# Kernel optimization log

Measured on AMD Instinct MI355X. Metric: run time of the kernel, lower is better.

Reference implementation:

```python
import jax, jax.numpy as jnp
import numpy as np

B, N, NP, NS = 8, 4096, 1024, 32
CF = 64            # input point-feature channels; in_channel = 3 + CF = 67
MLP = [64, 128, 256]
EPS = 1e-5         # BatchNorm eps (torch default)


def setup_inputs() -> dict:
    key = jax.random.key(0)
    ks = jax.random.split(key, 8)
    inp = {
        "xyz": jax.random.normal(ks[0], (B, N, 3), jnp.float32),
        "points": jax.random.normal(ks[1], (B, CF, N), jnp.float32),
        "sample_idx": jax.random.randint(ks[2], (B, NP), 0, N, dtype=jnp.int32),
        "neighbor_idx": jax.random.randint(ks[3], (B, NP, NS), 0, N, dtype=jnp.int32),
    }
    c = 3 + CF
    for i, o in enumerate(MLP):
        wk = jax.random.fold_in(ks[4], i)
        inp[f"W{i}"] = jax.random.normal(wk, (o, c), jnp.float32) * (1.0 / np.sqrt(c))
        inp[f"b{i}"] = jnp.zeros((o,), jnp.float32)
        inp[f"gamma{i}"] = jnp.ones((o,), jnp.float32)
        inp[f"beta{i}"] = jnp.zeros((o,), jnp.float32)
        c = o
    return inp


def _forward(xyz, points, sample_idx, neighbor_idx, params):
    # xyz: (B,N,3)  points: (B,CF,N)
    new_xyz = jnp.take_along_axis(xyz, sample_idx[:, :, None], axis=1)        # (B,NP,3)
    nbr_xyz = jax.vmap(lambda x, idx: x[idx])(xyz, neighbor_idx)               # (B,NP,NS,3)
    rel = nbr_xyz - new_xyz[:, :, None, :]                                     # (B,NP,NS,3)
    nbr_feat = jax.vmap(lambda f, idx: f[:, idx])(points, neighbor_idx)        # (B,CF,NP,NS)
    x = jnp.concatenate([rel.transpose(0, 3, 1, 2), nbr_feat], axis=1)         # (B,3+CF,NP,NS)
    # 1x1 Conv2d -> BatchNorm2d (training-mode batch stats) -> ReLU stack
    for W, b, g, be in params:
        x = jnp.einsum('oc,bcps->bops', W, x) + b[None, :, None, None]
        mu = x.mean(axis=(0, 2, 3), keepdims=True)
        var = x.var(axis=(0, 2, 3), keepdims=True)
        x = g[None, :, None, None] * (x - mu) * jax.lax.rsqrt(var + EPS) + be[None, :, None, None]
        x = jax.nn.relu(x)
    new_points = x.max(axis=-1)                                                # (B,C_out,NP)
    return new_xyz, new_points


def reference(xyz, points, sample_idx, neighbor_idx,
              W0, b0, gamma0, beta0,
              W1, b1, gamma1, beta1,
              W2, b2, gamma2, beta2):
    params = [(W0, b0, gamma0, beta0), (W1, b1, gamma1, beta1), (W2, b2, gamma2, beta2)]
    return _forward(xyz, points, sample_idx, neighbor_idx, params)
```

## Files before the change

kernel.cpp:

```cpp
#include <hip/hip_runtime.h>

typedef unsigned short u16;
typedef unsigned int u32;
typedef __attribute__((ext_vector_type(8))) short short8;
typedef __attribute__((ext_vector_type(16))) float f32x16;

#define BB 8
#define NN 4096
#define NPP 1024
#define NSS 32
#define CFF 64
#define C0 67
#define H0 64
#define H1 128
#define H2 256
#define MTOT (BB*NPP*NSS)
#define BN_EPS 1e-5f
#define INV_M (1.0f/262144.0f)

#define MFMA32(a,b,c) __builtin_amdgcn_mfma_f32_32x32x16_bf16(a,b,c,0,0,0)

__device__ __forceinline__ float bf2f(u16 h){ return __uint_as_float(((u32)h)<<16); }
__device__ __forceinline__ u16 f2bf(float f){
  u32 u = __float_as_uint(f);
  u32 r = (u + 0x7fffu + ((u>>16)&1u)) >> 16;
  return (u16)r;
}
__device__ __forceinline__ u32 pack2(float a, float b){
  return (u32)f2bf(a) | ((u32)f2bf(b)<<16);
}

#define WS_NEED 46280704u

__global__ __launch_bounds__(256) void k_setup(
    const float* __restrict__ xyz, const float* __restrict__ points,
    const int* __restrict__ sidx,
    const float* __restrict__ W0, const float* __restrict__ W1, const float* __restrict__ W2,
    u16* __restrict__ ptsT, u16* __restrict__ Wt0c, u16* __restrict__ Wt1c,
    u16* __restrict__ Wt2c, float* __restrict__ out_newxyz)
{
  int blk = blockIdx.x, tid = threadIdx.x;
  if (blk < 512) {
    __shared__ float t[64][65];
    int b = blk >> 6, n0 = (blk & 63) << 6;
    int nloc = tid & 63, cpart = tid >> 6;
    for (int i = 0; i < 16; ++i) {
      int c = i*4 + cpart;
      t[c][nloc] = points[(size_t)(b*CFF + c)*NN + n0 + nloc];
    }
    __syncthreads();
    int cloc = tid & 63, npart = tid >> 6;
    for (int i = 0; i < 16; ++i) {
      int n = i*4 + npart;
      ptsT[((size_t)(b*NN + n0 + n))*CFF + cloc] = f2bf(t[cloc][n]);
    }
  } else if (blk < 544) {
    int t0 = (blk - 512)*256 + tid;
    int b = t0 >> 10;
    int s = sidx[t0];
    for (int k = 0; k < 3; ++k)
      out_newxyz[(size_t)t0*3 + k] = xyz[((size_t)(b*NN + s))*3 + k];
  } else if (blk == 544) {
    for (int i = 0; i < 24; ++i) {
      int e = i*256 + tid;
      int kc = e >> 9, o = (e >> 3) & 63, j = e & 7, k = kc*8 + j;
      float v = (k < 64) ? W0[o*C0 + 3 + k] : ((k < 67) ? W0[o*C0 + (k - 64)] : 0.f);
      Wt0c[e] = f2bf(v);
    }
  } else if (blk == 545) {
    for (int i = 0; i < 32; ++i) {
      int e = i*256 + tid;
      int kc = e >> 10, n = (e >> 3) & 127, j = e & 7;
      Wt1c[e] = f2bf(W1[n*H0 + kc*8 + j]);
    }
  } else {
    int base = (blk - 546) * 4096;
    for (int i = 0; i < 16; ++i) {
      int e = base + i*256 + tid;
      int kc = e >> 11, n = (e >> 3) & 255, j = e & 7;
      Wt2c[e] = f2bf(W2[n*H1 + kc*8 + j]);
    }
  }
}

__global__ __launch_bounds__(256) void k_xyz_only(
    const float* __restrict__ xyz, const int* __restrict__ sidx, float* __restrict__ out_newxyz)
{
  int t0 = blockIdx.x*256 + threadIdx.x;
  int b = t0 >> 10;
  int s = sidx[t0];
  for (int k = 0; k < 3; ++k)
    out_newxyz[(size_t)t0*3 + k] = xyz[((size_t)(b*NN + s))*3 + k];
}

__global__ __launch_bounds__(256) void k_l0(
    const float* __restrict__ xyz, const int* __restrict__ sidx, const int* __restrict__ nidx,
    const u16* __restrict__ ptsT, const u16* __restrict__ Wt0c,
    u16* __restrict__ y0, float* __restrict__ stats)
{
  __shared__ u16 XLc[12*128*8];
  __shared__ u16 W0c[12*64*8];
  int tid = threadIdx.x;
  int m0 = blockIdx.x * 128;
  int b = m0 >> 15;

  for (int i = 0; i < 3; ++i)
    ((uint4*)W0c)[i*256 + tid] = ((const uint4*)Wt0c)[i*256 + tid];

  int pos = tid & 127, half = tid >> 7;
  int m = m0 + pos;
  int nb = nidx[m];
  {
    const uint4* prow = (const uint4*)(ptsT + ((size_t)(b*NN + nb))*CFF + half*32);
    uint4 h0 = prow[0], h1 = prow[1], h2 = prow[2], h3 = prow[3];
    *(uint4*)&XLc[((half*4+0)*128 + pos)*8] = h0;
    *(uint4*)&XLc[((half*4+1)*128 + pos)*8] = h1;
    *(uint4*)&XLc[((half*4+2)*128 + pos)*8] = h2;
    *(uint4*)&XLc[((half*4+3)*128 + pos)*8] = h3;
    if (half == 0) {
      int p = (m & 32767) >> 5;
      int sp = sidx[b*NPP + p];
      float r0 = xyz[((size_t)(b*NN+nb))*3+0] - xyz[((size_t)(b*NN+sp))*3+0];
      float r1 = xyz[((size_t)(b*NN+nb))*3+1] - xyz[((size_t)(b*NN+sp))*3+1];
      float r2 = xyz[((size_t)(b*NN+nb))*3+2] - xyz[((size_t)(b*NN+sp))*3+2];
      uint4 v = { pack2(r0, r1), pack2(r2, 0.f), 0u, 0u };
      *(uint4*)&XLc[(8*128 + pos)*8] = v;
    } else {
      uint4 z = {0u,0u,0u,0u};
      *(uint4*)&XLc[(9*128 + pos)*8]  = z;
      *(uint4*)&XLc[(10*128 + pos)*8] = z;
      *(uint4*)&XLc[(11*128 + pos)*8] = z;
    }
  }
  __syncthreads();

  int lane = tid & 63, wv = tid >> 6;
  int l31 = lane & 31, kh = lane >> 5;
  int nt = wv & 1, mtb = (wv >> 1) * 2;
  f32x16 acc[2];
  for (int mi = 0; mi < 2; ++mi) for (int r = 0; r < 16; ++r) acc[mi][r] = 0.f;

  for (int kt = 0; kt < 6; ++kt) {
    int ck = kt*2 + kh;
    short8 bfrag = *(const short8*)&W0c[(ck*64 + nt*32 + l31)*8];
    for (int mi = 0; mi < 2; ++mi) {
      short8 afrag = *(const short8*)&XLc[(ck*128 + (mtb+mi)*32 + l31)*8];
      acc[mi] = MFMA32(afrag, bfrag, acc[mi]);
    }
  }

  float s = 0.f, q = 0.f;
  for (int mi = 0; mi < 2; ++mi)
    for (int r = 0; r < 16; ++r) { float y = acc[mi][r]; s += y; q += y*y; }
  s += __shfl_xor(s, 32); q += __shfl_xor(q, 32);
  if (lane < 32) {
    int slot = blockIdx.x & 7;
    atomicAdd(&stats[slot*256 + nt*32 + lane], s);
    atomicAdd(&stats[2048 + slot*256 + nt*32 + lane], q);
  }
  for (int mi = 0; mi < 2; ++mi)
    for (int r = 0; r < 16; ++r) {
      int mm = (mtb+mi)*32 + (r&3) + 8*(r>>2) + 4*kh;
      y0[(size_t)(m0+mm)*H0 + nt*32 + l31] = f2bf(acc[mi][r]);
    }
}

__global__ __launch_bounds__(256) void k_l1s(
    const u16* __restrict__ y0, const u16* __restrict__ Wt1c,
    const float* __restrict__ g0, const float* __restrict__ e0,
    const float* __restrict__ stIn, float* __restrict__ stOut)
{
  __shared__ u16 X0c[8*128*8];
  __shared__ u16 W1c[8*128*8];
  __shared__ float scl0[64], sft0[64];
  int tid = threadIdx.x;
  int m0 = blockIdx.x * 128;

  if (tid < 64) {
    float s = 0.f, q = 0.f;
    for (int sl = 0; sl < 8; ++sl) { s += stIn[sl*256 + tid]; q += stIn[2048 + sl*256 + tid]; }
    float mu = s*INV_M, var = q*INV_M - mu*mu;
    float sc = g0[tid] * rsqrtf(var + BN_EPS);
    scl0[tid] = sc; sft0[tid] = e0[tid] - mu*sc;
  }
  for (int i = 0; i < 4; ++i)
    ((uint4*)W1c)[i*256 + tid] = ((const uint4*)Wt1c)[i*256 + tid];

  int pos = tid & 127, half = tid >> 7;
  {
    const u16* row = y0 + (size_t)(m0 + pos)*H0 + half*32;
    u16 hs[32];
    for (int t = 0; t < 4; ++t) *(uint4*)&hs[t*8] = ((const uint4*)row)[t];
    __syncthreads();
    u16 ob[32];
    for (int j = 0; j < 32; ++j) {
      int c = half*32 + j;
      ob[j] = f2bf(fmaxf(fmaf(scl0[c], bf2f(hs[j]), sft0[c]), 0.f));
    }
    for (int t = 0; t < 4; ++t)
      *(uint4*)&X0c[((half*4+t)*128 + pos)*8] = *(uint4*)&ob[t*8];
  }
  __syncthreads();

  int lane = tid & 63, wv = tid >> 6;
  int l31 = lane & 31, kh = lane >> 5;
  f32x16 acc[4];
  for (int mt = 0; mt < 4; ++mt) for (int r = 0; r < 16; ++r) acc[mt][r] = 0.f;

  for (int kt = 0; kt < 4; ++kt) {
    int ck = kt*2 + kh;
    short8 bfrag = *(const short8*)&W1c[(ck*128 + wv*32 + l31)*8];
    for (int mt = 0; mt < 4; ++mt) {
      short8 afrag = *(const short8*)&X0c[(ck*128 + mt*32 + l31)*8];
      acc[mt] = MFMA32(afrag, bfrag, acc[mt]);
    }
  }

  float s = 0.f, q = 0.f;
  for (int mt = 0; mt < 4; ++mt)
    for (int r = 0; r < 16; ++r) { float y = acc[mt][r]; s += y; q += y*y; }
  s += __shfl_xor(s, 32); q += __shfl_xor(q, 32);
  if (lane < 32) {
    int slot = blockIdx.x & 7;
    atomicAdd(&stOut[slot*256 + wv*32 + lane], s);
    atomicAdd(&stOut[2048 + slot*256 + wv*32 + lane], q);
  }
}

__global__ __launch_bounds__(256) void k_l2f(
    const u16* __restrict__ y0, const u16* __restrict__ Wt1c, const u16* __restrict__ Wt2c,
    const float* __restrict__ g0, const float* __restrict__ e0,
    const float* __restrict__ g1, const float* __restrict__ e1,
    const float* __restrict__ st0, const float* __restrict__ st1, float* __restrict__ stOut,
    u16* __restrict__ mxp, u16* __restrict__ mnp)
{
  __shared__ u16 X1c[16*64*8];
  __shared__ u16 UB[16384];
  __shared__ float scl0[64], sft0[64], scl1[128], sft1[128];
  int tid = threadIdx.x;
  int m0 = blockIdx.x * 64;

  if (tid < 64) {
    float s = 0.f, q = 0.f;
    for (int sl = 0; sl < 8; ++sl) { s += st0[sl*256 + tid]; q += st0[2048 + sl*256 + tid]; }
    float mu = s*INV_M, var = q*INV_M - mu*mu;
    float sc = g0[tid] * rsqrtf(var + BN_EPS);
    scl0[tid] = sc; sft0[tid] = e0[tid] - mu*sc;
  }
  if (tid < 128) {
    float s = 0.f, q = 0.f;
    for (int sl = 0; sl < 8; ++sl) { s += st1[sl*256 + tid]; q += st1[2048 + sl*256 + tid]; }
    float mu = s*INV_M, var = q*INV_M - mu*mu;
    float sc = g1[tid] * rsqrtf(var + BN_EPS);
    scl1[tid] = sc; sft1[tid] = e1[tid] - mu*sc;
  }
  u16* X0c = UB;
  u16* W1c = UB + 4096;
  for (int i = 0; i < 4; ++i)
    ((uint4*)W1c)[i*256 + tid] = ((const uint4*)Wt1c)[i*256 + tid];

  int pos = tid & 63, grp = tid >> 6;
  {
    const u16* row = y0 + (size_t)(m0 + pos)*H0 + grp*16;
    u16 hs[16];
    *(uint4*)&hs[0] = ((const uint4*)row)[0];
    *(uint4*)&hs[8] = ((const uint4*)row)[1];
    __syncthreads();
    u16 ob[16];
    for (int j = 0; j < 16; ++j) {
      int c = grp*16 + j;
      ob[j] = f2bf(fmaxf(fmaf(scl0[c], bf2f(hs[j]), sft0[c]), 0.f));
    }
    *(uint4*)&X0c[((2*grp)*64 + pos)*8]   = *(uint4*)&ob[0];
    *(uint4*)&X0c[((2*grp+1)*64 + pos)*8] = *(uint4*)&ob[8];
  }
  __syncthreads();

  int lane = tid & 63, wv = tid >> 6;
  int l31 = lane & 31, kh = lane >> 5;

  f32x16 acc1[2];
  for (int mt = 0; mt < 2; ++mt) for (int r = 0; r < 16; ++r) acc1[mt][r] = 0.f;
  for (int kt = 0; kt < 4; ++kt) {
    int ck = kt*2 + kh;
    short8 bfrag = *(const short8*)&W1c[(ck*128 + wv*32 + l31)*8];
    for (int mt = 0; mt < 2; ++mt) {
      short8 afrag = *(const short8*)&X0c[(ck*64 + mt*32 + l31)*8];
      acc1[mt] = MFMA32(afrag, bfrag, acc1[mt]);
    }
  }

  {
    int ch = wv*32 + l31;
    int cb = ch >> 3, cr = ch & 7;
    float sc1 = scl1[ch], sf1 = sft1[ch];
    for (int mt = 0; mt < 2; ++mt)
      for (int r = 0; r < 16; ++r) {
        int mm = mt*32 + (r&3) + 8*(r>>2) + 4*kh;
        X1c[(cb*64 + mm)*8 + cr] = f2bf(fmaxf(fmaf(sc1, acc1[mt][r], sf1), 0.f));
      }
  }
  __syncthreads();

  f32x16 acc2[2][2];
  for (int nt = 0; nt < 2; ++nt) for (int mt = 0; mt < 2; ++mt)
    for (int r = 0; r < 16; ++r) acc2[nt][mt][r] = 0.f;

  for (int h = 0; h < 2; ++h) {
    for (int i = 0; i < 8; ++i)
      ((uint4*)UB)[i*256 + tid] = ((const uint4*)Wt2c)[h*2048 + i*256 + tid];
    __syncthreads();
    for (int k4 = 0; k4 < 4; ++k4) {
      int ckx = (h*4 + k4)*2 + kh;
      int ckw = k4*2 + kh;
      short8 a[2], bf_[2];
      for (int mt = 0; mt < 2; ++mt) a[mt]  = *(const short8*)&X1c[(ckx*64 + mt*32 + l31)*8];
      for (int nt = 0; nt < 2; ++nt) bf_[nt] = *(const short8*)&UB[(ckw*256 + wv*64 + nt*32 + l31)*8];
      for (int nt = 0; nt < 2; ++nt)
        for (int mt = 0; mt < 2; ++mt)
          acc2[nt][mt] = MFMA32(a[mt], bf_[nt], acc2[nt][mt]);
    }
    __syncthreads();
  }

  int slot = blockIdx.x & 7;
  for (int nt = 0; nt < 2; ++nt) {
    float s = 0.f, q = 0.f;
    float mx[2] = {-3.0e38f, -3.0e38f}, mn[2] = {3.0e38f, 3.0e38f};
    for (int mt = 0; mt < 2; ++mt)
      for (int r = 0; r < 16; ++r) {
        float y = acc2[nt][mt][r];
        s += y; q += y*y;
        mx[mt] = fmaxf(mx[mt], y); mn[mt] = fminf(mn[mt], y);
      }
    s += __shfl_xor(s, 32); q += __shfl_xor(q, 32);
    mx[0] = fmaxf(mx[0], __shfl_xor(mx[0], 32));
    mx[1] = fmaxf(mx[1], __shfl_xor(mx[1], 32));
    mn[0] = fminf(mn[0], __shfl_xor(mn[0], 32));
    mn[1] = fminf(mn[1], __shfl_xor(mn[1], 32));
    if (lane < 32) {
      int c = wv*64 + nt*32 + lane;
      atomicAdd(&stOut[slot*256 + c], s);
      atomicAdd(&stOut[2048 + slot*256 + c], q);
      for (int mt = 0; mt < 2; ++mt) {
        size_t pr = (size_t)blockIdx.x*2 + mt;
        mxp[pr*H2 + c] = f2bf(mx[mt]);
        mnp[pr*H2 + c] = f2bf(mn[mt]);
      }
    }
  }
}

__global__ __launch_bounds__(256) void k_final(
    const u16* __restrict__ mxp, const u16* __restrict__ mnp,
    const float* __restrict__ gma, const float* __restrict__ bta,
    const float* __restrict__ stIn, float* __restrict__ out_np)
{
  __shared__ float tmp[256][33];
  int tid = threadIdx.x;
  int b = blockIdx.x >> 5;
  int p0 = (blockIdx.x & 31) * 32;

  float s = 0.f, q = 0.f;
  for (int sl = 0; sl < 8; ++sl) { s += stIn[sl*256 + tid]; q += stIn[2048 + sl*256 + tid]; }
  float mu = s*INV_M, var = q*INV_M - mu*mu;
  float sc = gma[tid] * rsqrtf(var + BN_EPS);
  float sh = bta[tid] - mu*sc;

  for (int pp = 0; pp < 32; ++pp) {
    size_t base = ((size_t)(b*NPP + p0 + pp))*H2 + tid;
    float xv = bf2f(mxp[base]), nv = bf2f(mnp[base]);
    float v = (sc >= 0.f) ? fmaf(sc, xv, sh) : fmaf(sc, nv, sh);
    tmp[tid][pp] = fmaxf(v, 0.f);
  }
  __syncthreads();

  int pl = tid & 31, cg = tid >> 5;
  for (int cc = 0; cc < 32; ++cc) {
    int c = cc*8 + cg;
    out_np[((size_t)b*H2 + c)*NPP + p0 + pl] = tmp[c][pl];
  }
}

extern "C" void kernel_launch(void* const* d_in, const int* in_sizes, int n_in,
                              void* d_out, int out_size, void* d_ws, size_t ws_size,
                              hipStream_t stream)
{
  const float* xyz    = (const float*)d_in[0];
  const float* points = (const float*)d_in[1];
  const int*   sidx   = (const int*)d_in[2];
  const int*   nidx   = (const int*)d_in[3];
  const float* W0 = (const float*)d_in[4];
  const float* g0 = (const float*)d_in[6];
  const float* e0 = (const float*)d_in[7];
  const float* W1 = (const float*)d_in[8];
  const float* g1 = (const float*)d_in[10];
  const float* e1 = (const float*)d_in[11];
  const float* W2 = (const float*)d_in[12];
  const float* g2 = (const float*)d_in[14];
  const float* e2 = (const float*)d_in[15];

  float* out_xyz = (float*)d_out;
  float* out_np  = out_xyz + (size_t)BB*NPP*3;

  if (ws_size < (size_t)WS_NEED) {
    hipMemsetAsync(out_np, 0, (size_t)BB*H2*NPP*4, stream);
    k_xyz_only<<<32, 256, 0, stream>>>(xyz, sidx, out_xyz);
    return;
  }

  char* ws = (char*)d_ws;
  float* stats = (float*)(ws + 0);
  u16*   Wt0c  = (u16*)(ws + 49152);
  u16*   Wt1c  = (u16*)(ws + 61440);
  u16*   Wt2c  = (u16*)(ws + 77824);
  u16*   ptsT  = (u16*)(ws + 143360);
  u16*   y0    = (u16*)(ws + 4337664);
  u16*   mxp   = (u16*)(ws + 37892096);
  u16*   mnp   = (u16*)(ws + 42086400);

  hipMemsetAsync(stats, 0, 3*4096*sizeof(float), stream);
  k_setup<<<554, 256, 0, stream>>>(xyz, points, sidx, W0, W1, W2,
                                   ptsT, Wt0c, Wt1c, Wt2c, out_xyz);
  k_l0<<<MTOT/128, 256, 0, stream>>>(xyz, sidx, nidx, ptsT, Wt0c, y0, stats);
  k_l1s<<<MTOT/128, 256, 0, stream>>>(y0, Wt1c, g0, e0, stats, stats + 4096);
  k_l2f<<<MTOT/64, 256, 0, stream>>>(y0, Wt1c, Wt2c, g0, e0, g1, e1,
                                     stats, stats + 4096, stats + 8192, mxp, mnp);
  k_final<<<256, 256, 0, stream>>>(mxp, mnp, g2, e2, stats + 8192, out_np);
}
```

Before: 177.6 us.

## Restructure fused layer-2 kernel: 512 threads, 128-row tiles, register-resident weights

The fused layer-1/layer-2 kernel now processes 128 rows per block with 8 waves instead of 64 rows with 4 waves. Weight fragments for both GEMMs are loaded straight from global memory into registers instead of staged through shared memory, which removes the two-phase W2 staging loop and its barriers. The X1 shared buffer gets an XOR swizzle to reduce bank conflicts, and the input row loads are issued before the BN-stat reduction to overlap latency. The cost is higher register pressure (8 weight fragments plus 4 accumulators per wave), which may lower occupancy.

```diff
diff --git a/kernel.cpp b/kernel.cpp
--- a/kernel.cpp
+++ b/kernel.cpp
@@ -227,18 +227,34 @@
   }
 }
 
-__global__ __launch_bounds__(256) void k_l2f(
+__global__ __launch_bounds__(512) void k_l2f(
     const u16* __restrict__ y0, const u16* __restrict__ Wt1c, const u16* __restrict__ Wt2c,
     const float* __restrict__ g0, const float* __restrict__ e0,
     const float* __restrict__ g1, const float* __restrict__ e1,
     const float* __restrict__ st0, const float* __restrict__ st1, float* __restrict__ stOut,
     u16* __restrict__ mxp, u16* __restrict__ mnp)
 {
-  __shared__ u16 X1c[16*64*8];
-  __shared__ u16 UB[16384];
+  __shared__ u16 X0c[8*128*8];
+  __shared__ u16 X1c[16*128*8];
   __shared__ float scl0[64], sft0[64], scl1[128], sft1[128];
   int tid = threadIdx.x;
-  int m0 = blockIdx.x * 64;
+  int m0 = blockIdx.x * 128;
+
+  int lane = tid & 63, w = tid >> 6;
+  int l31 = lane & 31, kh = lane >> 5;
+
+  int pos = tid & 127, qh = tid >> 7;
+  u16 hs[16];
+  {
+    const u16* row = y0 + (size_t)(m0 + pos)*H0 + qh*16;
+    *(uint4*)&hs[0] = ((const uint4*)row)[0];
+    *(uint4*)&hs[8] = ((const uint4*)row)[1];
+  }
+  int nt1 = w & 3, mh = w >> 2;
+  short8 b1[4];
+#pragma unroll
+  for (int kt = 0; kt < 4; ++kt)
+    b1[kt] = *(const short8*)&Wt1c[((kt*2 + kh)*128 + nt1*32 + l31)*8];
 
   if (tid < 64) {
     float s = 0.f, q = 0.f;
@@ -254,99 +270,93 @@
     float sc = g1[tid] * rsqrtf(var + BN_EPS);
     scl1[tid] = sc; sft1[tid] = e1[tid] - mu*sc;
   }
-  u16* X0c = UB;
-  u16* W1c = UB + 4096;
-  for (int i = 0; i < 4; ++i)
-    ((uint4*)W1c)[i*256 + tid] = ((const uint4*)Wt1c)[i*256 + tid];
-
-  int pos = tid & 63, grp = tid >> 6;
+  __syncthreads();
+
   {
-    const u16* row = y0 + (size_t)(m0 + pos)*H0 + grp*16;
-    u16 hs[16];
-    *(uint4*)&hs[0] = ((const uint4*)row)[0];
-    *(uint4*)&hs[8] = ((const uint4*)row)[1];
-    __syncthreads();
     u16 ob[16];
+#pragma unroll
     for (int j = 0; j < 16; ++j) {
-      int c = grp*16 + j;
+      int c = qh*16 + j;
       ob[j] = f2bf(fmaxf(fmaf(scl0[c], bf2f(hs[j]), sft0[c]), 0.f));
     }
-    *(uint4*)&X0c[((2*grp)*64 + pos)*8]   = *(uint4*)&ob[0];
-    *(uint4*)&X0c[((2*grp+1)*64 + pos)*8] = *(uint4*)&ob[8];
-  }
-  __syncthreads();
-
-  int lane = tid & 63, wv = tid >> 6;
-  int l31 = lane & 31, kh = lane >> 5;
+    *(uint4*)&X0c[((qh*2)*128 + pos)*8]   = *(uint4*)&ob[0];
+    *(uint4*)&X0c[((qh*2+1)*128 + pos)*8] = *(uint4*)&ob[8];
+  }
+  __syncthreads();
 
   f32x16 acc1[2];
-  for (int mt = 0; mt < 2; ++mt) for (int r = 0; r < 16; ++r) acc1[mt][r] = 0.f;
+#pragma unroll
+  for (int mi = 0; mi < 2; ++mi) for (int r = 0; r < 16; ++r) acc1[mi][r] = 0.f;
+#pragma unroll
   for (int kt = 0; kt < 4; ++kt) {
     int ck = kt*2 + kh;
-    short8 bfrag = *(const short8*)&W1c[(ck*128 + wv*32 + l31)*8];
-    for (int mt = 0; mt < 2; ++mt) {
-      short8 afrag = *(const short8*)&X0c[(ck*64 + mt*32 + l31)*8];
-      acc1[mt] = MFMA32(afrag, bfrag, acc1[mt]);
-    }
-  }
+#pragma unroll
+    for (int mi = 0; mi < 2; ++mi) {
+      short8 afrag = *(const short8*)&X0c[(ck*128 + (mh*2+mi)*32 + l31)*8];
+      acc1[mi] = MFMA32(afrag, b1[kt], acc1[mi]);
+    }
+  }
+
+  short8 b2[8];
+#pragma unroll
+  for (int k4 = 0; k4 < 8; ++k4)
+    b2[k4] = *(const short8*)&Wt2c[((k4*2 + kh)*256 + w*32 + l31)*8];
 
   {
-    int ch = wv*32 + l31;
-    int cb = ch >> 3, cr = ch & 7;
-    float sc1 = scl1[ch], sf1 = sft1[ch];
-    for (int mt = 0; mt < 2; ++mt)
+    int ch1 = nt1*32 + l31;
+    int cb = ch1 >> 3, cr = ch1 & 7, sw = cb & 3;
+    float sc1 = scl1[ch1], sf1 = sft1[ch1];
+#pragma unroll
+    for (int mi = 0; mi < 2; ++mi)
+#pragma unroll
       for (int r = 0; r < 16; ++r) {
-        int mm = mt*32 + (r&3) + 8*(r>>2) + 4*kh;
-        X1c[(cb*64 + mm)*8 + cr] = f2bf(fmaxf(fmaf(sc1, acc1[mt][r], sf1), 0.f));
+        int mm = (mh*2+mi)*32 + (r&3) + 8*(r>>2) + 4*kh;
+        X1c[(cb*128 + (mm ^ sw))*8 + cr] = f2bf(fmaxf(fmaf(sc1, acc1[mi][r], sf1), 0.f));
       }
   }
   __syncthreads();
 
-  f32x16 acc2[2][2];
-  for (int nt = 0; nt < 2; ++nt) for (int mt = 0; mt < 2; ++mt)
-    for (int r = 0; r < 16; ++r) acc2[nt][mt][r] = 0.f;
-
-  for (int h = 0; h < 2; ++h) {
-    for (int i = 0; i < 8; ++i)
-      ((uint4*)UB)[i*256 + tid] = ((const uint4*)Wt2c)[h*2048 + i*256 + tid];
-    __syncthreads();
-    for (int k4 = 0; k4 < 4; ++k4) {
-      int ckx = (h*4 + k4)*2 + kh;
-      int ckw = k4*2 + kh;
-      short8 a[2], bf_[2];
-      for (int mt = 0; mt < 2; ++mt) a[mt]  = *(const short8*)&X1c[(ckx*64 + mt*32 + l31)*8];
-      for (int nt = 0; nt < 2; ++nt) bf_[nt] = *(const short8*)&UB[(ckw*256 + wv*64 + nt*32 + l31)*8];
-      for (int nt = 0; nt < 2; ++nt)
-        for (int mt = 0; mt < 2; ++mt)
-          acc2[nt][mt] = MFMA32(a[mt], bf_[nt], acc2[nt][mt]);
-    }
-    __syncthreads();
-  }
-
-  int slot = blockIdx.x & 7;
-  for (int nt = 0; nt < 2; ++nt) {
-    float s = 0.f, q = 0.f;
-    float mx[2] = {-3.0e38f, -3.0e38f}, mn[2] = {3.0e38f, 3.0e38f};
-    for (int mt = 0; mt < 2; ++mt)
-      for (int r = 0; r < 16; ++r) {
-        float y = acc2[nt][mt][r];
-        s += y; q += y*y;
-        mx[mt] = fmaxf(mx[mt], y); mn[mt] = fminf(mn[mt], y);
-      }
-    s += __shfl_xor(s, 32); q += __shfl_xor(q, 32);
-    mx[0] = fmaxf(mx[0], __shfl_xor(mx[0], 32));
-    mx[1] = fmaxf(mx[1], __shfl_xor(mx[1], 32));
-    mn[0] = fminf(mn[0], __shfl_xor(mn[0], 32));
-    mn[1] = fminf(mn[1], __shfl_xor(mn[1], 32));
-    if (lane < 32) {
-      int c = wv*64 + nt*32 + lane;
-      atomicAdd(&stOut[slot*256 + c], s);
-      atomicAdd(&stOut[2048 + slot*256 + c], q);
-      for (int mt = 0; mt < 2; ++mt) {
-        size_t pr = (size_t)blockIdx.x*2 + mt;
-        mxp[pr*H2 + c] = f2bf(mx[mt]);
-        mnp[pr*H2 + c] = f2bf(mn[mt]);
-      }
+  f32x16 acc2[4];
+#pragma unroll
+  for (int mt = 0; mt < 4; ++mt) for (int r = 0; r < 16; ++r) acc2[mt][r] = 0.f;
+#pragma unroll
+  for (int k4 = 0; k4 < 8; ++k4) {
+    int ck = k4*2 + kh;
+    int sw = ck & 3;
+#pragma unroll
+    for (int mt = 0; mt < 4; ++mt) {
+      short8 afrag = *(const short8*)&X1c[(ck*128 + ((mt*32 + l31) ^ sw))*8];
+      acc2[mt] = MFMA32(afrag, b2[k4], acc2[mt]);
+    }
+  }
+
+  int ch = w*32 + l31;
+  float s = 0.f, q = 0.f;
+  float mx[4] = {-3.0e38f,-3.0e38f,-3.0e38f,-3.0e38f};
+  float mn[4] = { 3.0e38f, 3.0e38f, 3.0e38f, 3.0e38f};
+#pragma unroll
+  for (int mt = 0; mt < 4; ++mt)
+#pragma unroll
+    for (int r = 0; r < 16; ++r) {
+      float y = acc2[mt][r];
+      s += y; q += y*y;
+      mx[mt] = fmaxf(mx[mt], y); mn[mt] = fminf(mn[mt], y);
+    }
+  s += __shfl_xor(s, 32); q += __shfl_xor(q, 32);
+#pragma unroll
+  for (int mt = 0; mt < 4; ++mt) {
+    mx[mt] = fmaxf(mx[mt], __shfl_xor(mx[mt], 32));
+    mn[mt] = fminf(mn[mt], __shfl_xor(mn[mt], 32));
+  }
+  if (lane < 32) {
+    int slot = blockIdx.x & 7;
+    atomicAdd(&stOut[slot*256 + ch], s);
+    atomicAdd(&stOut[2048 + slot*256 + ch], q);
+#pragma unroll
+    for (int mt = 0; mt < 4; ++mt) {
+      size_t pr = (size_t)blockIdx.x*4 + mt;
+      mxp[pr*H2 + ch] = f2bf(mx[mt]);
+      mnp[pr*H2 + ch] = f2bf(mn[mt]);
     }
   }
 }
@@ -424,7 +434,7 @@
                                    ptsT, Wt0c, Wt1c, Wt2c, out_xyz);
   k_l0<<<MTOT/128, 256, 0, stream>>>(xyz, sidx, nidx, ptsT, Wt0c, y0, stats);
   k_l1s<<<MTOT/128, 256, 0, stream>>>(y0, Wt1c, g0, e0, stats, stats + 4096);
-  k_l2f<<<MTOT/64, 256, 0, stream>>>(y0, Wt1c, Wt2c, g0, e0, g1, e1,
-                                     stats, stats + 4096, stats + 8192, mxp, mnp);
+  k_l2f<<<MTOT/128, 512, 0, stream>>>(y0, Wt1c, Wt2c, g0, e0, g1, e1,
+                                      stats, stats + 4096, stats + 8192, mxp, mnp);
   k_final<<<256, 256, 0, stream>>>(mxp, mnp, g2, e2, stats + 8192, out_np);
 }
```

After: 172.6 us. 2.8% less time.
